# Optimization experiments

Hardware: AMD Instinct MI355X
Metric: run time of the kernel (lower is better)

## Reference

```python
import jax, jax.numpy as jnp
import numpy as np

EMBED_DIM = 1024
NUM_HEADS = 16
BATCH = 4
SEQ = 2048
HEAD_DIM = EMBED_DIM // NUM_HEADS


def get_alibi_slope(num_heads):
    x = (2 ** 8) ** (1 / num_heads)
    slope = jnp.array([1 / x ** (i + 1) for i in range(num_heads)], dtype=jnp.float32)
    return slope[:, None, None]  # [H,1,1]


def setup_inputs() -> dict:
    key = jax.random.key(0)
    k1, k2, k3 = jax.random.split(key, 3)
    x = jax.random.normal(k1, (BATCH, SEQ, EMBED_DIM), dtype=jnp.float32)
    # causal mask, broadcastable to [B,H,S,S]
    mask = jnp.tril(jnp.ones((SEQ, SEQ), dtype=bool))[None, None, :, :]
    W_qkv = jax.random.normal(k2, (EMBED_DIM, 3 * EMBED_DIM), dtype=jnp.float32) * (EMBED_DIM ** -0.5)
    b_qkv = jnp.zeros((3 * EMBED_DIM,), dtype=jnp.float32)
    W_out = jax.random.normal(k3, (EMBED_DIM, EMBED_DIM), dtype=jnp.float32) * (EMBED_DIM ** -0.5)
    b_out = jnp.zeros((EMBED_DIM,), dtype=jnp.float32)
    return {"x": x, "mask": mask, "W_qkv": W_qkv, "b_qkv": b_qkv, "W_out": W_out, "b_out": b_out}


def reference(x, mask, W_qkv, b_qkv, W_out, b_out):
    B, S, E = x.shape
    H, D = NUM_HEADS, HEAD_DIM
    qkv = x @ W_qkv + b_qkv                     # [B,S,3E]
    qkv = qkv.reshape(B, S, 3, H, D)
    q, k, v = qkv[:, :, 0], qkv[:, :, 1], qkv[:, :, 2]  # each [B,S,H,D]
    scores = jnp.einsum('bqhd,bkhd->bhqk', q, k) / jnp.sqrt(jnp.asarray(D, x.dtype))
    # ALiBi bias: slope[h] * (k_pos - q_pos)
    rel = (jnp.arange(S)[None, :] - jnp.arange(S)[:, None]).astype(x.dtype)  # [S,S]
    scores = scores + get_alibi_slope(H).astype(x.dtype) * rel               # broadcast [H,S,S]
    scores = jnp.where(mask, scores, jnp.asarray(-1e9, x.dtype))
    attn = jax.nn.softmax(scores, axis=-1)       # [B,H,S,S]
    out = jnp.einsum('bhqk,bkhd->bqhd', attn, v).reshape(B, S, E)
    return out @ W_out + b_out
```

## Files before the change

kernel.cpp:

```cpp
#include <hip/hip_runtime.h>
#include <hip/hip_bf16.h>
#include <cstdint>
#include <cstddef>

#define BATCH  4
#define SEQ    2048
#define EMBED  1024
#define NHEADS 16
#define HDIM   64

typedef __attribute__((ext_vector_type(8))) short  short8;
typedef __attribute__((ext_vector_type(4))) float  floatx4;

#define MASK_NEG (-1.0e30f)
#define LOG2E    1.44269504f

__device__ __forceinline__ float bf2f(ushort u) {
  union { uint32_t i; float f; } v; v.i = ((uint32_t)u) << 16; return v.f;
}
__device__ __forceinline__ ushort f2bf(float f) {
  union { float f; uint32_t i; } v; v.f = f;
  uint32_t u = v.i;
  return (ushort)((u + 0x7fffu + ((u >> 16) & 1u)) >> 16);
}
__device__ __forceinline__ uint32_t f2bf_pk(float a, float b) {
  union { __hip_bfloat162 h; uint32_t u; } v;
  v.h = __float22bfloat162_rn(make_float2(a, b));
  return v.u;
}
__device__ __forceinline__ float fast_exp2(float x) {
  float r;
  asm("v_exp_f32 %0, %1" : "=v"(r) : "v"(x));
  return r;
}
__device__ __forceinline__ floatx4 max4(floatx4 a, floatx4 b) {
  floatx4 r;
  r[0] = fmaxf(a[0], b[0]); r[1] = fmaxf(a[1], b[1]);
  r[2] = fmaxf(a[2], b[2]); r[3] = fmaxf(a[3], b[3]);
  return r;
}
__device__ __forceinline__ void gll16(const ushort* g, ushort* l) {
  __builtin_amdgcn_global_load_lds(
      (const __attribute__((address_space(1))) void*)g,
      (__attribute__((address_space(3))) void*)l, 16, 0, 0);
}

__global__ __launch_bounds__(256) void detect_dtype(
    const uint32_t* __restrict__ x, int* __restrict__ flag) {
  __shared__ int sh[256];
  int tid = threadIdx.x;
  int c = 0;
#pragma unroll
  for (int i = 0; i < 16; i++) {
    uint32_t w = x[tid * 16 + i];
    uint32_t lo = w & 0xFFFFu;
    int e = (int)((lo >> 7) & 0xFF);
    if (lo == 0u || (e >= 100 && e <= 140)) c++;
  }
  sh[tid] = c;
  __syncthreads();
  if (tid == 0) {
    int s = 0;
    for (int i = 0; i < 256; i++) s += sh[i];
    *flag = (s >= 3500) ? 1 : 0;
  }
}

__global__ __launch_bounds__(256) void cvt_bf16_v4(
    const void* __restrict__ in, ushort* __restrict__ out,
    const int* __restrict__ flag, int n4) {
  bool isbf = (*flag != 0);
  int stride = gridDim.x * 256;
  for (int i = blockIdx.x * 256 + threadIdx.x; i < n4; i += stride) {
    if (isbf) {
      ((uint2*)out)[i] = ((const uint2*)in)[i];
    } else {
      float4 f = ((const float4*)in)[i];
      uint2 o;
      o.x = f2bf_pk(f.x, f.y);
      o.y = f2bf_pk(f.z, f.w);
      ((uint2*)out)[i] = o;
    }
  }
}

__global__ __launch_bounds__(256) void cvt_biases(
    const void* __restrict__ bq, const void* __restrict__ bo,
    ushort* __restrict__ bqb, ushort* __restrict__ bob,
    const int* __restrict__ flag) {
  bool isbf = (*flag != 0);
  int i = blockIdx.x * 256 + threadIdx.x;
  if (i < 3 * EMBED) {
    bqb[i] = isbf ? ((const ushort*)bq)[i] : f2bf(((const float*)bq)[i]);
  } else {
    int j = i - 3 * EMBED;
    bob[j] = isbf ? ((const ushort*)bo)[j] : f2bf(((const float*)bo)[j]);
  }
}

__global__ __launch_bounds__(256) void transpose_cvt(
    const void* __restrict__ in, ushort* __restrict__ out,
    const int* __restrict__ flag, int R, int C) {
  bool isbf = (*flag != 0);
  __shared__ ushort tile[32][33];
  int bx = blockIdx.x * 32;
  int by = blockIdx.y * 32;
  int tx = threadIdx.x & 31, ty = threadIdx.x >> 5;
#pragma unroll
  for (int i = 0; i < 32; i += 8) {
    size_t idx = (size_t)(by + ty + i) * C + bx + tx;
    tile[ty + i][tx] = isbf ? ((const ushort*)in)[idx] : f2bf(((const float*)in)[idx]);
  }
  __syncthreads();
#pragma unroll
  for (int i = 0; i < 32; i += 8)
    out[(size_t)(bx + ty + i) * R + by + tx] = tile[tx][ty + i];
}

__global__ __launch_bounds__(256) void transpose_v(
    const ushort* __restrict__ in, ushort* __restrict__ out) {
  __shared__ ushort tile[32][33];
  int bh = blockIdx.z;
  int s0 = blockIdx.x * 32;
  int d0 = blockIdx.y * 32;
  int tx = threadIdx.x & 31, ty = threadIdx.x >> 5;
  const ushort* ip = in + (size_t)bh * SEQ * HDIM;
  ushort* op = out + (size_t)bh * SEQ * HDIM;
#pragma unroll
  for (int i = 0; i < 32; i += 8)
    tile[ty + i][tx] = ip[(size_t)(s0 + ty + i) * HDIM + d0 + tx];
  __syncthreads();
#pragma unroll
  for (int i = 0; i < 32; i += 8)
    op[(size_t)(d0 + ty + i) * SEQ + s0 + tx] = tile[tx][ty + i];
}

template <int EPI>
__global__ __launch_bounds__(256) void gemm128(
    const ushort* __restrict__ A, const ushort* __restrict__ BT,
    const ushort* __restrict__ bias,
    ushort* __restrict__ out0, ushort* __restrict__ out1, ushort* __restrict__ out2,
    const int* __restrict__ flag,
    int M, int N, int K) {
  __shared__ __align__(16) ushort Al[128 * 64];
  __shared__ __align__(16) ushort Bl[128 * 64];

  const int tid  = threadIdx.x;
  const int lane = tid & 63, wave = tid >> 6;
  const int quad = lane >> 4, l15 = lane & 15;
  const int wm = wave >> 1, wn = wave & 1;

  const int Lb  = blockIdx.y * gridDim.x + blockIdx.x;
  const int xcd = Lb & 7, ib = Lb >> 3;
  const int cpx = gridDim.x >> 3;
  const int bx  = xcd * cpx + (ib % cpx);
  const int by  = ib / cpx;
  const int rowA0 = by * 128;
  const int colB0 = bx * 128;

  floatx4 acc[4][4] = {};

  int srow[4], sc8[4];
#pragma unroll
  for (int j = 0; j < 4; j++) {
    int s = tid + j * 256;
    srow[j] = s >> 3;
    sc8[j] = ((s & 7) ^ (srow[j] & 7)) * 8;
  }

  for (int kk = 0; kk < K; kk += 64) {
    __syncthreads();
#pragma unroll
    for (int j = 0; j < 4; j++)
      gll16(&A[(size_t)(rowA0 + srow[j]) * K + kk + sc8[j]], &Al[(tid + j * 256) * 8]);
#pragma unroll
    for (int j = 0; j < 4; j++)
      gll16(&BT[(size_t)(colB0 + srow[j]) * K + kk + sc8[j]], &Bl[(tid + j * 256) * 8]);
    __syncthreads();

#pragma unroll
    for (int h = 0; h < 2; h++) {
      short8 af[4], bf[4];
#pragma unroll
      for (int mt = 0; mt < 4; mt++) {
        int row = wm * 64 + mt * 16 + l15;
        int pos = (quad + 4 * h) ^ (l15 & 7);
        af[mt] = *(const short8*)&Al[row * 64 + pos * 8];
      }
#pragma unroll
      for (int nt = 0; nt < 4; nt++) {
        int row = wn * 64 + nt * 16 + l15;
        int pos = (quad + 4 * h) ^ (l15 & 7);
        bf[nt] = *(const short8*)&Bl[row * 64 + pos * 8];
      }
#pragma unroll
      for (int mt = 0; mt < 4; mt++)
#pragma unroll
        for (int nt = 0; nt < 4; nt++)
          acc[mt][nt] = __builtin_amdgcn_mfma_f32_16x16x32_bf16(af[mt], bf[nt], acc[mt][nt], 0, 0, 0);
    }
  }

  const bool isbf = (EPI == 1) ? (*flag != 0) : true;

#pragma unroll
  for (int mt = 0; mt < 4; mt++)
#pragma unroll
    for (int nt = 0; nt < 4; nt++)
#pragma unroll
      for (int r = 0; r < 4; r++) {
        int row = rowA0 + wm * 64 + mt * 16 + quad * 4 + r;
        int col = colB0 + wn * 64 + nt * 16 + l15;
        float v = acc[mt][nt][r] + bf2f(bias[col]);
        if (EPI == 0) {
          int three = col >> 10, rem = col & 1023, h = rem >> 6, d = rem & 63;
          int b = row >> 11, s = row & 2047;
          ushort* dst = (three == 0) ? out0 : (three == 1) ? out1 : out2;
          dst[((size_t)(b * NHEADS + h) * SEQ + s) * HDIM + d] = f2bf(v);
        } else {
          if (isbf) out0[(size_t)row * N + col] = f2bf(v);
          else      ((float*)out0)[(size_t)row * N + col] = v;
        }
      }
}

__global__ __launch_bounds__(256, 4) void attn_kernel(
    const ushort* __restrict__ Q, const ushort* __restrict__ K,
    const ushort* __restrict__ VT, ushort* __restrict__ Oout) {
  __shared__ __align__(16) ushort Kl[2][64 * 64];
  __shared__ __align__(16) ushort Vt[2][64 * 64];
  __shared__ __align__(16) ushort Pl[4][16 * 64];

  const int tid  = threadIdx.x;
  const int lane = tid & 63, wave = tid >> 6;
  const int quad = lane >> 4, l15 = lane & 15;

  const int L   = blockIdx.x + 16 * blockIdx.y + 256 * blockIdx.z;
  const int xcd = L & 7;
  const int idx = L >> 3;
  const int bh  = xcd * 8 + (idx >> 4);
  const int p   = idx & 15;
  const int h   = bh & 15, b = bh >> 4;

  const ushort* Qp  = Q  + (size_t)bh * SEQ * HDIM;
  const ushort* Kp  = K  + (size_t)bh * SEQ * HDIM;
  const ushort* VTp = VT + (size_t)bh * SEQ * HDIM;

  const float slope2 = exp2f(-0.5f * (float)(h + 1)) * LOG2E;
  const float c2 = 0.125f * LOG2E;

  floatx4 ab[4];
#pragma unroll
  for (int kct = 0; kct < 4; kct++)
#pragma unroll
    for (int r = 0; r < 4; r++)
      ab[kct][r] = slope2 * (float)(kct * 16 + quad * 4 + r);

  const int sr0 = tid >> 3, sr1 = sr0 + 32;
  const int sc  = tid & 7;
  const int so  = sc * 8;
  const int sw0 = sr0 * 64 + (sc ^ (sr0 & 7)) * 8;
  const int sw1 = sr1 * 64 + (sc ^ (sr0 & 7)) * 8;
  const int sxr = l15 & 7;

#define ATTN_TILE(KB, CUR, MASKED)                                            \
  do {                                                                        \
    floatx4 w[4];                                                             \
    _Pragma("unroll")                                                         \
    for (int kct = 0; kct < 4; kct++) {                                       \
      const ushort* kr = &Kl[CUR][(kct * 16 + l15) * 64];                     \
      short8 a0 = *(const short8*)&kr[(quad ^ sxr) * 8];                      \
      short8 a1 = *(const short8*)&kr[((quad + 4) ^ sxr) * 8];                \
      floatx4 z = {};                                                         \
      z = __builtin_amdgcn_mfma_f32_16x16x32_bf16(a0, qf0, z, 0, 0, 0);       \
      z = __builtin_amdgcn_mfma_f32_16x16x32_bf16(a1, qf1, z, 0, 0, 0);       \
      w[kct] = z * c2 + ab[kct];                                              \
    }                                                                         \
    if (MASKED) {                                                             \
      const float qrel = qrowf - (float)(KB);                                 \
      _Pragma("unroll")                                                       \
      for (int kct = 0; kct < 4; kct++)                                       \
        _Pragma("unroll")                                                     \
        for (int r = 0; r < 4; r++)                                           \
          if ((float)(kct * 16 + quad * 4 + r) > qrel) w[kct][r] = MASK_NEG;  \
    }                                                                         \
    floatx4 wm4 = max4(max4(w[0], w[1]), max4(w[2], w[3]));                   \
    float mloc = fmaxf(fmaxf(wm4[0], wm4[1]), fmaxf(wm4[2], wm4[3]));         \
    mloc = fmaxf(mloc, __shfl_xor(mloc, 16, 64));                             \
    mloc = fmaxf(mloc, __shfl_xor(mloc, 32, 64));                             \
    const float bk = slope2 * (float)(KB);                                    \
    const float mlt = mloc + bk;                                              \
    const unsigned long long g = __ballot(mlt > m2 + 8.0f);                   \
    float al = 1.0f;                                                          \
    if (g) {                                                                  \
      float mn = fmaxf(m2, mlt);                                              \
      al = fast_exp2(m2 - mn);                                                \
      m2 = mn;                                                                \
    }                                                                         \
    const float mnb = m2 - bk;                                                \
    float rs = 0.f;                                                           \
    _Pragma("unroll")                                                         \
    for (int kct = 0; kct < 4; kct++) {                                       \
      float p0 = fast_exp2(w[kct][0] - mnb);                                  \
      float p1 = fast_exp2(w[kct][1] - mnb);                                  \
      float p2 = fast_exp2(w[kct][2] - mnb);                                  \
      float p3 = fast_exp2(w[kct][3] - mnb);                                  \
      rs += (p0 + p1) + (p2 + p3);                                            \
      uint2 pw;                                                               \
      pw.x = f2bf_pk(p0, p1);                                                 \
      pw.y = f2bf_pk(p2, p3);                                                 \
      *(uint2*)&Pl[wave][l15 * 64 + ((kct * 2 + (quad >> 1)) ^ sxr) * 8 +     \
                         (quad & 1) * 4] = pw;                                \
    }                                                                         \
    if (g) {                                                                  \
      floatx4 alrv;                                                           \
      _Pragma("unroll")                                                       \
      for (int r = 0; r < 4; r++) alrv[r] = __shfl(al, quad * 4 + r, 16);     \
      _Pragma("unroll")                                                       \
      for (int ct = 0; ct < 4; ct++) o_acc[ct] *= alrv;                       \
      li = li * al + rs;                                                      \
    } else {                                                                  \
      li += rs;                                                               \
    }                                                                         \
    _Pragma("unroll")                                                         \
    for (int ks = 0; ks < 2; ks++) {                                          \
      short8 vf[4];                                                           \
      _Pragma("unroll")                                                       \
      for (int ct = 0; ct < 4; ct++)                                          \
        vf[ct] = *(const short8*)&Vt[CUR][(ct * 16 + l15) * 64 +              \
                                          ((ks * 4 + quad) ^ sxr) * 8];       \
      short8 pf = *(const short8*)&Pl[wave][l15 * 64 +                        \
                                            ((ks * 4 + quad) ^ sxr) * 8];     \
      _Pragma("unroll")                                                       \
      for (int ct = 0; ct < 4; ct++)                                          \
        o_acc[ct] = __builtin_amdgcn_mfma_f32_16x16x32_bf16(pf, vf[ct],       \
                                                            o_acc[ct], 0, 0, 0); \
    }                                                                         \
  } while (0)

  for (int qsel = 0; qsel < 2; qsel++) {
    const int qt  = qsel ? (31 - p) : p;
    const int wq0 = qt * 64 + wave * 16;

    short8 qf0, qf1;
    {
      const ushort* qr = &Qp[(size_t)(wq0 + l15) * HDIM];
      qf0 = *(const short8*)&qr[quad * 8];
      qf1 = *(const short8*)&qr[32 + quad * 8];
    }

    float m2 = MASK_NEG, li = 0.f;
    const float qrowf = (float)(wq0 + l15);
    floatx4 o_acc[4] = {};

    uint4 pk0 = *(const uint4*)&Kp[(size_t)sr0 * HDIM + so];
    uint4 pk1 = *(const uint4*)&Kp[(size_t)sr1 * HDIM + so];
    uint4 pv0 = *(const uint4*)&VTp[(size_t)sr0 * SEQ + so];
    uint4 pv1 = *(const uint4*)&VTp[(size_t)sr1 * SEQ + so];
    __syncthreads();
    *(uint4*)&Kl[0][sw0] = pk0;
    *(uint4*)&Kl[0][sw1] = pk1;
    *(uint4*)&Vt[0][sw0] = pv0;
    *(uint4*)&Vt[0][sw1] = pv1;
    __syncthreads();

    const int last = qt;
    for (int kt = 0; kt < last; kt++) {
      const int kb = kt * 64;
      const int cur = kt & 1;

      {
        const int kb2 = kb + 64;
        pk0 = *(const uint4*)&Kp[(size_t)(kb2 + sr0) * HDIM + so];
        pk1 = *(const uint4*)&Kp[(size_t)(kb2 + sr1) * HDIM + so];
        pv0 = *(const uint4*)&VTp[(size_t)sr0 * SEQ + kb2 + so];
        pv1 = *(const uint4*)&VTp[(size_t)sr1 * SEQ + kb2 + so];
      }

      ATTN_TILE(kb, cur, 0);

      {
        const int nxt = cur ^ 1;
        *(uint4*)&Kl[nxt][sw0] = pk0;
        *(uint4*)&Kl[nxt][sw1] = pk1;
        *(uint4*)&Vt[nxt][sw0] = pv0;
        *(uint4*)&Vt[nxt][sw1] = pv1;
      }
      __syncthreads();
    }

    ATTN_TILE(last * 64, last & 1, 1);

    {
      float lif = li + __shfl_xor(li, 16, 64);
      lif += __shfl_xor(lif, 32, 64);
      float inv = 1.0f / fmaxf(lif, 1e-20f);
      float invr[4];
#pragma unroll
      for (int r = 0; r < 4; r++) invr[r] = __shfl(inv, quad * 4 + r, 16);
#pragma unroll
      for (int ct = 0; ct < 4; ct++)
#pragma unroll
        for (int r = 0; r < 4; r++) {
          int q = wq0 + quad * 4 + r;
          float v = o_acc[ct][r] * invr[r];
          Oout[(size_t)(b * SEQ + q) * EMBED + h * HDIM + ct * 16 + l15] = f2bf(v);
        }
    }
  }
#undef ATTN_TILE
}

extern "C" void kernel_launch(void* const* d_in, const int* in_sizes, int n_in,
                              void* d_out, int out_size, void* d_ws, size_t ws_size,
                              hipStream_t stream) {
  const void* x     = d_in[0];
  const void* W_qkv = d_in[2];
  const void* b_qkv = d_in[3];
  const void* W_out = d_in[4];
  const void* b_out = d_in[5];

  char* ws = (char*)d_ws;
  int*    flag = (int*)(ws + 0);
  ushort* xb   = (ushort*)(ws + 1024);
  ushort* WTq  = (ushort*)(ws + 16778240);
  ushort* WTo  = (ushort*)(ws + 23069696);
  ushort* bqb  = (ushort*)(ws + 25166848);
  ushort* bob  = (ushort*)(ws + 25172992);
  ushort* Kw   = (ushort*)(ws + 25175040);
  ushort* Vw   = (ushort*)(ws + 41952256);
  ushort* VTw  = (ushort*)(ws + 58729472);
  ushort* Aw   = Vw;
  ushort* Qw   = (ws_size >= (size_t)75506688 + 16777216)
                   ? (ushort*)(ws + 75506688)
                   : (ushort*)d_out;

  detect_dtype<<<1, 256, 0, stream>>>((const uint32_t*)x, flag);

  cvt_bf16_v4<<<2048, 256, 0, stream>>>(x, xb, flag, BATCH * SEQ * EMBED / 4);
  cvt_biases<<<16, 256, 0, stream>>>(b_qkv, b_out, bqb, bob, flag);

  transpose_cvt<<<dim3(3072 / 32, 1024 / 32), 256, 0, stream>>>(W_qkv, WTq, flag, 1024, 3072);
  transpose_cvt<<<dim3(1024 / 32, 1024 / 32), 256, 0, stream>>>(W_out, WTo, flag, 1024, 1024);

  gemm128<0><<<dim3(3072 / 128, 8192 / 128), 256, 0, stream>>>(
      xb, WTq, bqb, Qw, Kw, Vw, flag, BATCH * SEQ, 3 * EMBED, EMBED);

  transpose_v<<<dim3(SEQ / 32, HDIM / 32, BATCH * NHEADS), 256, 0, stream>>>(Vw, VTw);

  attn_kernel<<<dim3(16, 16, 4), 256, 0, stream>>>(Qw, Kw, VTw, Aw);

  gemm128<1><<<dim3(1024 / 128, 8192 / 128), 256, 0, stream>>>(
      Aw, WTo, bob, (ushort*)d_out, nullptr, nullptr, flag, BATCH * SEQ, EMBED, EMBED);
}
```

Before: 307.1 us.

## Use 128-row query tiles with two M-fragments per wave in attention

Each attention block now handles one 128-row query tile, with each wave owning 32 query rows as two 16-row fragments, instead of two 64-row tiles paired for causal load balance. K fragments read from shared memory are reused across both query fragments, which halves LDS K/V traffic per query row and per synchronisation. Blocks are ordered longest-first. The cost is more registers, so launch bounds drop to 3 waves per SIMD, and the P staging buffer doubles. Load balance across blocks now relies on scheduling order rather than explicit pairing.

```diff
diff --git a/kernel.cpp b/kernel.cpp
--- a/kernel.cpp
+++ b/kernel.cpp
@@ -224,12 +224,12 @@
       }
 }
 
-__global__ __launch_bounds__(256, 4) void attn_kernel(
+__global__ __launch_bounds__(256, 3) void attn_kernel(
     const ushort* __restrict__ Q, const ushort* __restrict__ K,
     const ushort* __restrict__ VT, ushort* __restrict__ Oout) {
   __shared__ __align__(16) ushort Kl[2][64 * 64];
   __shared__ __align__(16) ushort Vt[2][64 * 64];
-  __shared__ __align__(16) ushort Pl[4][16 * 64];
+  __shared__ __align__(16) ushort Pl[4][32 * 64];
 
   const int tid  = threadIdx.x;
   const int lane = tid & 63, wave = tid >> 6;
@@ -239,7 +239,7 @@
   const int xcd = L & 7;
   const int idx = L >> 3;
   const int bh  = xcd * 8 + (idx >> 4);
-  const int p   = idx & 15;
+  const int qt  = 15 - (idx & 15);
   const int h   = bh & 15, b = bh >> 4;
 
   const ushort* Qp  = Q  + (size_t)bh * SEQ * HDIM;
@@ -263,64 +263,88 @@
   const int sw1 = sr1 * 64 + (sc ^ (sr0 & 7)) * 8;
   const int sxr = l15 & 7;
 
+  const int wq0 = qt * 128 + wave * 32;
+
+  short8 qf[2][2];
+#pragma unroll
+  for (int mf = 0; mf < 2; mf++) {
+    const ushort* qr = &Qp[(size_t)(wq0 + mf * 16 + l15) * HDIM];
+    qf[mf][0] = *(const short8*)&qr[quad * 8];
+    qf[mf][1] = *(const short8*)&qr[32 + quad * 8];
+  }
+
+  float m2s[2] = {MASK_NEG, MASK_NEG}, lis[2] = {0.f, 0.f};
+  float qrowf[2];
+#pragma unroll
+  for (int mf = 0; mf < 2; mf++) qrowf[mf] = (float)(wq0 + mf * 16 + l15);
+  floatx4 o_acc[2][4] = {};
+
 #define ATTN_TILE(KB, CUR, MASKED)                                            \
   do {                                                                        \
-    floatx4 w[4];                                                             \
+    short8 kfa[4], kfb[4];                                                    \
     _Pragma("unroll")                                                         \
     for (int kct = 0; kct < 4; kct++) {                                       \
       const ushort* kr = &Kl[CUR][(kct * 16 + l15) * 64];                     \
-      short8 a0 = *(const short8*)&kr[(quad ^ sxr) * 8];                      \
-      short8 a1 = *(const short8*)&kr[((quad + 4) ^ sxr) * 8];                \
-      floatx4 z = {};                                                         \
-      z = __builtin_amdgcn_mfma_f32_16x16x32_bf16(a0, qf0, z, 0, 0, 0);       \
-      z = __builtin_amdgcn_mfma_f32_16x16x32_bf16(a1, qf1, z, 0, 0, 0);       \
-      w[kct] = z * c2 + ab[kct];                                              \
+      kfa[kct] = *(const short8*)&kr[(quad ^ sxr) * 8];                       \
+      kfb[kct] = *(const short8*)&kr[((quad + 4) ^ sxr) * 8];                 \
     }                                                                         \
-    if (MASKED) {                                                             \
-      const float qrel = qrowf - (float)(KB);                                 \
+    _Pragma("unroll")                                                         \
+    for (int mf = 0; mf < 2; mf++) {                                          \
+      floatx4 w[4];                                                           \
       _Pragma("unroll")                                                       \
-      for (int kct = 0; kct < 4; kct++)                                       \
+      for (int kct = 0; kct < 4; kct++) {                                     \
+        floatx4 z = {};                                                       \
+        z = __builtin_amdgcn_mfma_f32_16x16x32_bf16(kfa[kct], qf[mf][0], z, 0, 0, 0); \
+        z = __builtin_amdgcn_mfma_f32_16x16x32_bf16(kfb[kct], qf[mf][1], z, 0, 0, 0); \
+        w[kct] = z * c2 + ab[kct];                                            \
+      }                                                                       \
+      if (MASKED) {                                                           \
+        const float qrel = qrowf[mf] - (float)(KB);                           \
         _Pragma("unroll")                                                     \
-        for (int r = 0; r < 4; r++)                                           \
-          if ((float)(kct * 16 + quad * 4 + r) > qrel) w[kct][r] = MASK_NEG;  \
-    }                                                                         \
-    floatx4 wm4 = max4(max4(w[0], w[1]), max4(w[2], w[3]));                   \
-    float mloc = fmaxf(fmaxf(wm4[0], wm4[1]), fmaxf(wm4[2], wm4[3]));         \
-    mloc = fmaxf(mloc, __shfl_xor(mloc, 16, 64));                             \
-    mloc = fmaxf(mloc, __shfl_xor(mloc, 32, 64));                             \
-    const float bk = slope2 * (float)(KB);                                    \
-    const float mlt = mloc + bk;                                              \
-    const unsigned long long g = __ballot(mlt > m2 + 8.0f);                   \
-    float al = 1.0f;                                                          \
-    if (g) {                                                                  \
-      float mn = fmaxf(m2, mlt);                                              \
-      al = fast_exp2(m2 - mn);                                                \
-      m2 = mn;                                                                \
-    }                                                                         \
-    const float mnb = m2 - bk;                                                \
-    float rs = 0.f;                                                           \
-    _Pragma("unroll")                                                         \
-    for (int kct = 0; kct < 4; kct++) {                                       \
-      float p0 = fast_exp2(w[kct][0] - mnb);                                  \
-      float p1 = fast_exp2(w[kct][1] - mnb);                                  \
-      float p2 = fast_exp2(w[kct][2] - mnb);                                  \
-      float p3 = fast_exp2(w[kct][3] - mnb);                                  \
-      rs += (p0 + p1) + (p2 + p3);                                            \
-      uint2 pw;                                                               \
-      pw.x = f2bf_pk(p0, p1);                                                 \
-      pw.y = f2bf_pk(p2, p3);                                                 \
-      *(uint2*)&Pl[wave][l15 * 64 + ((kct * 2 + (quad >> 1)) ^ sxr) * 8 +     \
-                         (quad & 1) * 4] = pw;                                \
-    }                                                                         \
-    if (g) {                                                                  \
-      floatx4 alrv;                                                           \
+        for (int kct = 0; kct < 4; kct++)                                     \
+          _Pragma("unroll")                                                   \
+          for (int r = 0; r < 4; r++)                                         \
+            if ((float)(kct * 16 + quad * 4 + r) > qrel) w[kct][r] = MASK_NEG;\
+      }                                                                       \
+      floatx4 wm4 = max4(max4(w[0], w[1]), max4(w[2], w[3]));                 \
+      float mloc = fmaxf(fmaxf(wm4[0], wm4[1]), fmaxf(wm4[2], wm4[3]));       \
+      mloc = fmaxf(mloc, __shfl_xor(mloc, 16, 64));                           \
+      mloc = fmaxf(mloc, __shfl_xor(mloc, 32, 64));                           \
+      const float bk = slope2 * (float)(KB);                                  \
+      const float mlt = mloc + bk;                                            \
+      const unsigned long long g = __ballot(mlt > m2s[mf] + 8.0f);            \
+      float al = 1.0f;                                                        \
+      if (g) {                                                                \
+        float mn = fmaxf(m2s[mf], mlt);                                       \
+        al = fast_exp2(m2s[mf] - mn);                                         \
+        m2s[mf] = mn;                                                         \
+      }                                                                       \
+      const float mnb = m2s[mf] - bk;                                         \
+      float rs = 0.f;                                                         \
       _Pragma("unroll")                                                       \
-      for (int r = 0; r < 4; r++) alrv[r] = __shfl(al, quad * 4 + r, 16);     \
-      _Pragma("unroll")                                                       \
-      for (int ct = 0; ct < 4; ct++) o_acc[ct] *= alrv;                       \
-      li = li * al + rs;                                                      \
-    } else {                                                                  \
-      li += rs;                                                               \
+      for (int kct = 0; kct < 4; kct++) {                                     \
+        float p0 = fast_exp2(w[kct][0] - mnb);                                \
+        float p1 = fast_exp2(w[kct][1] - mnb);                                \
+        float p2 = fast_exp2(w[kct][2] - mnb);                                \
+        float p3 = fast_exp2(w[kct][3] - mnb);                                \
+        rs += (p0 + p1) + (p2 + p3);                                          \
+        uint2 pw;                                                             \
+        pw.x = f2bf_pk(p0, p1);                                               \
+        pw.y = f2bf_pk(p2, p3);                                               \
+        *(uint2*)&Pl[wave][(mf * 16 + l15) * 64 +                             \
+                           ((kct * 2 + (quad >> 1)) ^ sxr) * 8 +              \
+                           (quad & 1) * 4] = pw;                              \
+      }                                                                       \
+      if (g) {                                                                \
+        floatx4 alrv;                                                         \
+        _Pragma("unroll")                                                     \
+        for (int r = 0; r < 4; r++) alrv[r] = __shfl(al, quad * 4 + r, 16);   \
+        _Pragma("unroll")                                                     \
+        for (int ct = 0; ct < 4; ct++) o_acc[mf][ct] *= alrv;                 \
+        lis[mf] = lis[mf] * al + rs;                                          \
+      } else {                                                                \
+        lis[mf] += rs;                                                        \
+      }                                                                       \
     }                                                                         \
     _Pragma("unroll")                                                         \
     for (int ks = 0; ks < 2; ks++) {                                          \
@@ -329,84 +353,92 @@
       for (int ct = 0; ct < 4; ct++)                                          \
         vf[ct] = *(const short8*)&Vt[CUR][(ct * 16 + l15) * 64 +              \
                                           ((ks * 4 + quad) ^ sxr) * 8];       \
-      short8 pf = *(const short8*)&Pl[wave][l15 * 64 +                        \
-                                            ((ks * 4 + quad) ^ sxr) * 8];     \
       _Pragma("unroll")                                                       \
-      for (int ct = 0; ct < 4; ct++)                                          \
-        o_acc[ct] = __builtin_amdgcn_mfma_f32_16x16x32_bf16(pf, vf[ct],       \
-                                                            o_acc[ct], 0, 0, 0); \
+      for (int mf = 0; mf < 2; mf++) {                                        \
+        short8 pf = *(const short8*)&Pl[wave][(mf * 16 + l15) * 64 +          \
+                                              ((ks * 4 + quad) ^ sxr) * 8];   \
+        _Pragma("unroll")                                                     \
+        for (int ct = 0; ct < 4; ct++)                                        \
+          o_acc[mf][ct] = __builtin_amdgcn_mfma_f32_16x16x32_bf16(            \
+              pf, vf[ct], o_acc[mf][ct], 0, 0, 0);                            \
+      }                                                                       \
     }                                                                         \
   } while (0)
 
-  for (int qsel = 0; qsel < 2; qsel++) {
-    const int qt  = qsel ? (31 - p) : p;
-    const int wq0 = qt * 64 + wave * 16;
-
-    short8 qf0, qf1;
+  uint4 pk0 = *(const uint4*)&Kp[(size_t)sr0 * HDIM + so];
+  uint4 pk1 = *(const uint4*)&Kp[(size_t)sr1 * HDIM + so];
+  uint4 pv0 = *(const uint4*)&VTp[(size_t)sr0 * SEQ + so];
+  uint4 pv1 = *(const uint4*)&VTp[(size_t)sr1 * SEQ + so];
+  *(uint4*)&Kl[0][sw0] = pk0;
+  *(uint4*)&Kl[0][sw1] = pk1;
+  *(uint4*)&Vt[0][sw0] = pv0;
+  *(uint4*)&Vt[0][sw1] = pv1;
+  __syncthreads();
+
+  const int nfull = 2 * qt;
+  for (int kt = 0; kt < nfull; kt++) {
+    const int kb = kt * 64;
+    const int cur = kt & 1;
+
     {
-      const ushort* qr = &Qp[(size_t)(wq0 + l15) * HDIM];
-      qf0 = *(const short8*)&qr[quad * 8];
-      qf1 = *(const short8*)&qr[32 + quad * 8];
+      const int kb2 = kb + 64;
+      pk0 = *(const uint4*)&Kp[(size_t)(kb2 + sr0) * HDIM + so];
+      pk1 = *(const uint4*)&Kp[(size_t)(kb2 + sr1) * HDIM + so];
+      pv0 = *(const uint4*)&VTp[(size_t)sr0 * SEQ + kb2 + so];
+      pv1 = *(const uint4*)&VTp[(size_t)sr1 * SEQ + kb2 + so];
     }
 
-    float m2 = MASK_NEG, li = 0.f;
-    const float qrowf = (float)(wq0 + l15);
-    floatx4 o_acc[4] = {};
-
-    uint4 pk0 = *(const uint4*)&Kp[(size_t)sr0 * HDIM + so];
-    uint4 pk1 = *(const uint4*)&Kp[(size_t)sr1 * HDIM + so];
-    uint4 pv0 = *(const uint4*)&VTp[(size_t)sr0 * SEQ + so];
-    uint4 pv1 = *(const uint4*)&VTp[(size_t)sr1 * SEQ + so];
+    ATTN_TILE(kb, cur, 0);
+
+    {
+      const int nxt = cur ^ 1;
+      *(uint4*)&Kl[nxt][sw0] = pk0;
+      *(uint4*)&Kl[nxt][sw1] = pk1;
+      *(uint4*)&Vt[nxt][sw0] = pv0;
+      *(uint4*)&Vt[nxt][sw1] = pv1;
+    }
     __syncthreads();
-    *(uint4*)&Kl[0][sw0] = pk0;
-    *(uint4*)&Kl[0][sw1] = pk1;
-    *(uint4*)&Vt[0][sw0] = pv0;
-    *(uint4*)&Vt[0][sw1] = pv1;
+  }
+
+  {
+    const int kb = nfull * 64;
+    const int cur = nfull & 1;
+    const int kb2 = kb + 64;
+    pk0 = *(const uint4*)&Kp[(size_t)(kb2 + sr0) * HDIM + so];
+    pk1 = *(const uint4*)&Kp[(size_t)(kb2 + sr1) * HDIM + so];
+    pv0 = *(const uint4*)&VTp[(size_t)sr0 * SEQ + kb2 + so];
+    pv1 = *(const uint4*)&VTp[(size_t)sr1 * SEQ + kb2 + so];
+
+    ATTN_TILE(kb, cur, 1);
+
+    const int nxt = cur ^ 1;
+    *(uint4*)&Kl[nxt][sw0] = pk0;
+    *(uint4*)&Kl[nxt][sw1] = pk1;
+    *(uint4*)&Vt[nxt][sw0] = pv0;
+    *(uint4*)&Vt[nxt][sw1] = pv1;
     __syncthreads();
-
-    const int last = qt;
-    for (int kt = 0; kt < last; kt++) {
-      const int kb = kt * 64;
-      const int cur = kt & 1;
-
-      {
-        const int kb2 = kb + 64;
-        pk0 = *(const uint4*)&Kp[(size_t)(kb2 + sr0) * HDIM + so];
-        pk1 = *(const uint4*)&Kp[(size_t)(kb2 + sr1) * HDIM + so];
-        pv0 = *(const uint4*)&VTp[(size_t)sr0 * SEQ + kb2 + so];
-        pv1 = *(const uint4*)&VTp[(size_t)sr1 * SEQ + kb2 + so];
+  }
+
+  if (wave & 2) {
+    ATTN_TILE((nfull + 1) * 64, (nfull + 1) & 1, 1);
+  }
+
+#pragma unroll
+  for (int mf = 0; mf < 2; mf++) {
+    float lif = lis[mf] + __shfl_xor(lis[mf], 16, 64);
+    lif += __shfl_xor(lif, 32, 64);
+    float inv = 1.0f / fmaxf(lif, 1e-20f);
+    float invr[4];
+#pragma unroll
+    for (int r = 0; r < 4; r++) invr[r] = __shfl(inv, quad * 4 + r, 16);
+#pragma unroll
+    for (int ct = 0; ct < 4; ct++)
+#pragma unroll
+      for (int r = 0; r < 4; r++) {
+        int q = wq0 + mf * 16 + quad * 4 + r;
+        float v = o_acc[mf][ct][r] * invr[r];
+        Oout[(size_t)(b * SEQ + q) * EMBED + h * HDIM + ct * 16 + l15] = f2bf(v);
       }
-
-      ATTN_TILE(kb, cur, 0);
-
-      {
-        const int nxt = cur ^ 1;
-        *(uint4*)&Kl[nxt][sw0] = pk0;
-        *(uint4*)&Kl[nxt][sw1] = pk1;
-        *(uint4*)&Vt[nxt][sw0] = pv0;
-        *(uint4*)&Vt[nxt][sw1] = pv1;
-      }
-      __syncthreads();
-    }
-
-    ATTN_TILE(last * 64, last & 1, 1);
-
-    {
-      float lif = li + __shfl_xor(li, 16, 64);
-      lif += __shfl_xor(lif, 32, 64);
-      float inv = 1.0f / fmaxf(lif, 1e-20f);
-      float invr[4];
-#pragma unroll
-      for (int r = 0; r < 4; r++) invr[r] = __shfl(inv, quad * 4 + r, 16);
-#pragma unroll
-      for (int ct = 0; ct < 4; ct++)
-#pragma unroll
-        for (int r = 0; r < 4; r++) {
-          int q = wq0 + quad * 4 + r;
-          float v = o_acc[ct][r] * invr[r];
-          Oout[(size_t)(b * SEQ + q) * EMBED + h * HDIM + ct * 16 + l15] = f2bf(v);
-        }
-    }
   }
 #undef ATTN_TILE
 }
```

Result: slower. 328.8 us (+7.1%).

## Use direct global-to-LDS loads for attention K/V staging; drop GEMM XCD swizzle

Applied to the files above, without the earlier changes.

The attention kernel now stages K and V tiles with direct global-to-LDS loads (gll16) instead of loading into registers and then writing to shared memory. The aim is to cut register pressure and the extra VGPR round-trip while keeping the double-buffer prefetch. Separately, the GEMM drops its XCD-aware block remapping and uses plain blockIdx tiles, which may reduce L2 locality per XCD. The swizzled source column now places the XOR pattern on the global side so the LDS write stays linear.

```diff
diff --git a/kernel.cpp b/kernel.cpp
--- a/kernel.cpp
+++ b/kernel.cpp
@@ -149,14 +149,8 @@
   const int lane = tid & 63, wave = tid >> 6;
   const int quad = lane >> 4, l15 = lane & 15;
   const int wm = wave >> 1, wn = wave & 1;
-
-  const int Lb  = blockIdx.y * gridDim.x + blockIdx.x;
-  const int xcd = Lb & 7, ib = Lb >> 3;
-  const int cpx = gridDim.x >> 3;
-  const int bx  = xcd * cpx + (ib % cpx);
-  const int by  = ib / cpx;
-  const int rowA0 = by * 128;
-  const int colB0 = bx * 128;
+  const int rowA0 = blockIdx.y * 128;
+  const int colB0 = blockIdx.x * 128;
 
   floatx4 acc[4][4] = {};
 
@@ -256,12 +250,17 @@
     for (int r = 0; r < 4; r++)
       ab[kct][r] = slope2 * (float)(kct * 16 + quad * 4 + r);
 
-  const int sr0 = tid >> 3, sr1 = sr0 + 32;
-  const int sc  = tid & 7;
-  const int so  = sc * 8;
-  const int sw0 = sr0 * 64 + (sc ^ (sr0 & 7)) * 8;
-  const int sw1 = sr1 * 64 + (sc ^ (sr0 & 7)) * 8;
+  const int sr0 = tid >> 3;
+  const int scc = ((tid & 7) ^ (sr0 & 7)) * 8;
   const int sxr = l15 & 7;
+
+#define STAGE(KB, BUF)                                                        \
+  do {                                                                        \
+    gll16(&Kp[(size_t)((KB) + sr0) * HDIM + scc],       &Kl[BUF][tid * 8]);   \
+    gll16(&Kp[(size_t)((KB) + sr0 + 32) * HDIM + scc],  &Kl[BUF][tid * 8 + 2048]); \
+    gll16(&VTp[(size_t)sr0 * SEQ + (KB) + scc],         &Vt[BUF][tid * 8]);   \
+    gll16(&VTp[(size_t)(sr0 + 32) * SEQ + (KB) + scc],  &Vt[BUF][tid * 8 + 2048]); \
+  } while (0)
 
 #define ATTN_TILE(KB, CUR, MASKED)                                            \
   do {                                                                        \
@@ -353,39 +352,15 @@
     const float qrowf = (float)(wq0 + l15);
     floatx4 o_acc[4] = {};
 
-    uint4 pk0 = *(const uint4*)&Kp[(size_t)sr0 * HDIM + so];
-    uint4 pk1 = *(const uint4*)&Kp[(size_t)sr1 * HDIM + so];
-    uint4 pv0 = *(const uint4*)&VTp[(size_t)sr0 * SEQ + so];
-    uint4 pv1 = *(const uint4*)&VTp[(size_t)sr1 * SEQ + so];
     __syncthreads();
-    *(uint4*)&Kl[0][sw0] = pk0;
-    *(uint4*)&Kl[0][sw1] = pk1;
-    *(uint4*)&Vt[0][sw0] = pv0;
-    *(uint4*)&Vt[0][sw1] = pv1;
+    STAGE(0, 0);
     __syncthreads();
 
     const int last = qt;
     for (int kt = 0; kt < last; kt++) {
-      const int kb = kt * 64;
       const int cur = kt & 1;
-
-      {
-        const int kb2 = kb + 64;
-        pk0 = *(const uint4*)&Kp[(size_t)(kb2 + sr0) * HDIM + so];
-        pk1 = *(const uint4*)&Kp[(size_t)(kb2 + sr1) * HDIM + so];
-        pv0 = *(const uint4*)&VTp[(size_t)sr0 * SEQ + kb2 + so];
-        pv1 = *(const uint4*)&VTp[(size_t)sr1 * SEQ + kb2 + so];
-      }
-
-      ATTN_TILE(kb, cur, 0);
-
-      {
-        const int nxt = cur ^ 1;
-        *(uint4*)&Kl[nxt][sw0] = pk0;
-        *(uint4*)&Kl[nxt][sw1] = pk1;
-        *(uint4*)&Vt[nxt][sw0] = pv0;
-        *(uint4*)&Vt[nxt][sw1] = pv1;
-      }
+      STAGE((kt + 1) * 64, cur ^ 1);
+      ATTN_TILE(kt * 64, cur, 0);
       __syncthreads();
     }
 
@@ -409,6 +384,7 @@
     }
   }
 #undef ATTN_TILE
+#undef STAGE
 }
 
 extern "C" void kernel_launch(void* const* d_in, const int* in_sizes, int n_in,
```

New measurement: 295.0 us. -3.9%, faster.
